# Performance work log

Hardware: AMD Instinct MI355X
Metric: run time of the kernel (lower is better)

## Reference

```python
import jax, jax.numpy as jnp
import numpy as np

EPS = 1e-8  # torch F.cosine_similarity norm clamp
TEMPERATURE = 0.05


def setup_inputs() -> dict:
    key = jax.random.key(0)
    k1, k2 = jax.random.split(key)
    N, D = 8192, 768
    query_embeddings = jax.random.normal(k1, (N, D), dtype=jnp.float32)
    content_embeddings = jax.random.normal(k2, (N, D), dtype=jnp.float32)
    return {"query_embeddings": query_embeddings, "content_embeddings": content_embeddings}


def reference(query_embeddings, content_embeddings):
    # cosine_similarity(q[:,None], c[None,:], dim=2) == normalize(q) @ normalize(c).T
    qn = query_embeddings / jnp.maximum(
        jnp.linalg.norm(query_embeddings, axis=-1, keepdims=True), EPS)
    cn = content_embeddings / jnp.maximum(
        jnp.linalg.norm(content_embeddings, axis=-1, keepdims=True), EPS)
    sim = jnp.einsum('nd,md->nm', qn, cn) / TEMPERATURE  # [N, N]
    # cross-entropy with targets = arange(N): positive is the diagonal
    logz = jax.nn.logsumexp(sim, axis=-1)                # [N]
    loss = jnp.mean(logz - jnp.diagonal(sim))
    return loss
```

## Files before the change

kernel.cpp:

```cpp
#include <hip/hip_runtime.h>
#include <hip/hip_bf16.h>


#define NROWS 8192
#define DDIM  768
#define ROWB  1536
#define FROWB 3072
#define BK 64
#define NKT  (DDIM / BK)
#define NIT  (NKT / 2)
#define GRID_T (NROWS / 256)

constexpr float INV_TEMP = 20.0f;
constexpr float NORM_EPS = 1e-8f;

using bf16 = __hip_bfloat16;
typedef __attribute__((ext_vector_type(4))) float  f32x4;
typedef __attribute__((ext_vector_type(8))) short  bf16x8;

__global__ void norm_diag_kernel(const float* __restrict__ q, const float* __restrict__ c,
                                 bf16* __restrict__ qn, bf16* __restrict__ cn,
                                 float* __restrict__ diag) {
    int row = blockIdx.x, t = threadIdx.x;
    const float4* qv = (const float4*)(q + (size_t)row * DDIM);
    const float4* cv = (const float4*)(c + (size_t)row * DDIM);
    float4 a = qv[t], b = cv[t];
    float ssq = a.x * a.x + a.y * a.y + a.z * a.z + a.w * a.w;
    float ssc = b.x * b.x + b.y * b.y + b.z * b.z + b.w * b.w;
    float dot = a.x * b.x + a.y * b.y + a.z * b.z + a.w * b.w;
    #pragma unroll
    for (int m = 32; m; m >>= 1) {
        ssq += __shfl_xor(ssq, m);
        ssc += __shfl_xor(ssc, m);
        dot += __shfl_xor(dot, m);
    }
    __shared__ float w3[3][4];
    if ((t & 63) == 0) { w3[t >> 6][0] = ssq; w3[t >> 6][1] = ssc; w3[t >> 6][2] = dot; }
    __syncthreads();
    float SSQ = w3[0][0] + w3[1][0] + w3[2][0];
    float SSC = w3[0][1] + w3[1][1] + w3[2][1];
    float DOT = w3[0][2] + w3[1][2] + w3[2][2];
    float invq = 1.0f / fmaxf(sqrtf(SSQ), NORM_EPS);
    float invc = 1.0f / fmaxf(sqrtf(SSC), NORM_EPS);
    if (t == 0) diag[row] = DOT * invq * invc * INV_TEMP;
    union { ushort4 u; bf16 h[4]; } oq, oc;
    oq.h[0] = __float2bfloat16(a.x * invq); oq.h[1] = __float2bfloat16(a.y * invq);
    oq.h[2] = __float2bfloat16(a.z * invq); oq.h[3] = __float2bfloat16(a.w * invq);
    oc.h[0] = __float2bfloat16(b.x * invc); oc.h[1] = __float2bfloat16(b.y * invc);
    oc.h[2] = __float2bfloat16(b.z * invc); oc.h[3] = __float2bfloat16(b.w * invc);
    ((ushort4*)(qn + (size_t)row * DDIM))[t] = oq.u;
    ((ushort4*)(cn + (size_t)row * DDIM))[t] = oc.u;
}

__device__ __forceinline__ void async16(void* l, const void* g) {
    __builtin_amdgcn_global_load_lds(
        (const __attribute__((address_space(1))) void*)g,
        (__attribute__((address_space(3))) void*)l, 16, 0, 0);
}

#define BARRIER __builtin_amdgcn_s_barrier()
#define SCHED0  __builtin_amdgcn_sched_barrier(0)
#define PRIO1   __builtin_amdgcn_s_setprio(1)
#define PRIO0   __builtin_amdgcn_s_setprio(0)
#define LGKM0   do { asm volatile("s_waitcnt lgkmcnt(0)" ::: "memory"); SCHED0; } while (0)
#define VMCNT(n) do { asm volatile("s_waitcnt vmcnt(" #n ")" ::: "memory"); SCHED0; } while (0)

#define STAGE_A(P, H, KT) do {                                              \
    const char* _g = aG + (size_t)(H) * 128 * ROWB + (size_t)(KT) * 128;    \
    char* _l = lds + (P) * 65536 + (H) * 16384 + dstW;                      \
    async16(_l, _g);                                                        \
    async16(_l + 8192, _g + 64 * ROWB);                                     \
} while (0)
#define STAGE_B(P, H, KT) do {                                              \
    const char* _g = bG + (size_t)(H) * 128 * ROWB + (size_t)(KT) * 128;    \
    char* _l = lds + 32768 + (P) * 65536 + (H) * 16384 + dstW;              \
    async16(_l, _g);                                                        \
    async16(_l + 8192, _g + 64 * ROWB);                                     \
} while (0)

#define READ_A(P, MH) do {                                                  \
    const char* _ab = lds + (P) * 65536 + aBaseT + (MH) * 64 * 128;         \
    _Pragma("unroll") for (int mi = 0; mi < 4; ++mi) {                      \
        a[mi][0] = *(const bf16x8*)(_ab + mi * 2048 + xk0);                 \
        a[mi][1] = *(const bf16x8*)(_ab + mi * 2048 + xk1);                 \
    }                                                                       \
} while (0)
#define READ_B(P, NH) do {                                                  \
    const char* _bb = lds + 32768 + (P) * 65536 + bBaseT + (NH) * 32 * 128; \
    _Pragma("unroll") for (int ni = 0; ni < 2; ++ni) {                      \
        bfr[NH][ni][0] = *(const bf16x8*)(_bb + ni * 2048 + xk0);           \
        bfr[NH][ni][1] = *(const bf16x8*)(_bb + ni * 2048 + xk1);           \
    }                                                                       \
} while (0)

#define MFMA_Q(MH, NH)                                                      \
    _Pragma("unroll") for (int mi = 0; mi < 4; ++mi)                        \
    _Pragma("unroll") for (int ni = 0; ni < 2; ++ni) {                      \
        acc[(MH)*4+mi][(NH)*2+ni] = __builtin_amdgcn_mfma_f32_16x16x32_bf16(\
            a[mi][0], bfr[NH][ni][0], acc[(MH)*4+mi][(NH)*2+ni], 0, 0, 0);  \
        acc[(MH)*4+mi][(NH)*2+ni] = __builtin_amdgcn_mfma_f32_16x16x32_bf16(\
            a[mi][1], bfr[NH][ni][1], acc[(MH)*4+mi][(NH)*2+ni], 0, 0, 0);  \
    }

__launch_bounds__(512, 2)
__global__ void simgemm_kernel(const bf16* __restrict__ A, const bf16* __restrict__ B,
                               float* __restrict__ partial) {
    __shared__ __attribute__((aligned(16))) char smem[131072];
    char* lds = smem;

    const int bid = blockIdx.x;
    const int tm = bid >> 5, tn = bid & 31;
    const int rowBase = tm * 256, colBase = tn * 256;
    const int tid = threadIdx.x;
    const int wid = tid >> 6, lane = tid & 63;
    const int wr = wid >> 2, wc = wid & 3;

    const int sr  = tid >> 3;
    const int scb = ((tid & 7) * 16) ^ ((sr & 7) << 4);
    const char* aG = (const char*)A + (size_t)(rowBase + sr) * ROWB + scb;
    const char* bG = (const char*)B + (size_t)(colBase + sr) * ROWB + scb;
    const int dstW = wid * 1024;

    const int aBaseT = wr * 16384 + (lane & 15) * 128;
    const int bBaseT = (wc >> 1) * 16384 + ((wc & 1) * 64 + (lane & 15)) * 128;
    const int klane  = (lane >> 4) * 16;
    const int swz    = (lane & 7) << 4;
    const int xk0    = klane ^ swz;
    const int xk1    = (64 + klane) ^ swz;

    f32x4  acc[8][4] = {};
    bf16x8 a[4][2];
    bf16x8 bfr[2][2][2];

    STAGE_A(0, 0, 0); STAGE_A(0, 1, 0);
    STAGE_B(0, 0, 0); STAGE_B(0, 1, 0);
    STAGE_A(1, 0, 1); STAGE_A(1, 1, 1);
    VMCNT(4);
    BARRIER; SCHED0;

    for (int i = 0; i < NIT; ++i) {
        const int t1 = 2 * i + 1;
        const int t2 = 2 * i + 2, t3 = 2 * i + 3;
        const bool more = (i + 1 < NIT);
        READ_A(0, 0); READ_B(0, 0);
        STAGE_B(1, 0, t1);
        BARRIER; LGKM0; PRIO1; MFMA_Q(0, 0); PRIO0; BARRIER; SCHED0;
        READ_B(0, 1);
        STAGE_B(1, 1, t1);
        BARRIER; LGKM0; PRIO1; MFMA_Q(0, 1); PRIO0; BARRIER; SCHED0;
        READ_A(0, 1);
        if (more) STAGE_A(0, 0, t2);
        BARRIER; LGKM0; PRIO1; MFMA_Q(1, 0); PRIO0; BARRIER; SCHED0;
        if (more) STAGE_A(0, 1, t2);
        BARRIER; LGKM0; PRIO1; MFMA_Q(1, 1); PRIO0;
        if (more) { VMCNT(4); } else { VMCNT(0); }
        BARRIER; SCHED0;
        READ_A(1, 0); READ_B(1, 0);
        if (more) STAGE_B(0, 0, t2);
        BARRIER; LGKM0; PRIO1; MFMA_Q(0, 0); PRIO0; BARRIER; SCHED0;
        READ_B(1, 1);
        if (more) STAGE_B(0, 1, t2);
        BARRIER; LGKM0; PRIO1; MFMA_Q(0, 1); PRIO0; BARRIER; SCHED0;
        READ_A(1, 1);
        if (more) STAGE_A(1, 0, t3);
        BARRIER; LGKM0; PRIO1; MFMA_Q(1, 0); PRIO0; BARRIER; SCHED0;
        if (more) STAGE_A(1, 1, t3);
        BARRIER; LGKM0; PRIO1; MFMA_Q(1, 1); PRIO0;
        if (more) { VMCNT(4); }
        BARRIER; SCHED0;
    }

    __syncthreads();
    float* red = (float*)smem;
    #pragma unroll
    for (int m = 0; m < 8; ++m) {
        #pragma unroll
        for (int r = 0; r < 4; ++r) {
            float s = 0.f;
            #pragma unroll
            for (int n = 0; n < 4; ++n)
                s += __expf(fmaf(INV_TEMP, acc[m][n][r], -INV_TEMP));
            s += __shfl_xor(s, 1);
            s += __shfl_xor(s, 2);
            s += __shfl_xor(s, 4);
            s += __shfl_xor(s, 8);
            if ((lane & 15) == 0)
                red[(wr * 128 + m * 16 + (lane >> 4) * 4 + r) * 4 + wc] = s;
        }
    }
    __syncthreads();
    if (tid < 256)
        partial[(size_t)(rowBase + tid) * GRID_T + tn] =
            red[tid * 4 + 0] + red[tid * 4 + 1] + red[tid * 4 + 2] + red[tid * 4 + 3];
}

__global__ void finalize_kernel(const float* __restrict__ partial,
                                const float* __restrict__ diag,
                                float* __restrict__ out) {
    int row = blockIdx.x * 256 + threadIdx.x;
    const float4* p = (const float4*)(partial + (size_t)row * GRID_T);
    float z = 0.f;
    #pragma unroll
    for (int i = 0; i < GRID_T / 4; ++i) {
        float4 v = p[i];
        z += v.x + v.y + v.z + v.w;
    }
    float term = INV_TEMP + logf(z) - diag[row];
    #pragma unroll
    for (int m = 32; m; m >>= 1) term += __shfl_xor(term, m);
    __shared__ float wsum[4];
    if ((threadIdx.x & 63) == 0) wsum[threadIdx.x >> 6] = term;
    __syncthreads();
    if (threadIdx.x == 0) {
        float s = wsum[0] + wsum[1] + wsum[2] + wsum[3];
        atomicAdd(out, s * (1.0f / NROWS));
    }
}

extern "C" void kernel_launch(void* const* d_in, const int* in_sizes, int n_in,
                              void* d_out, int out_size, void* d_ws, size_t ws_size,
                              hipStream_t stream) {
    const float* q = (const float*)d_in[0];
    const float* c = (const float*)d_in[1];
    float* out = (float*)d_out;

    char* ws = (char*)d_ws;
    bf16* qn = (bf16*)ws;
    bf16* cn = (bf16*)(ws + (size_t)NROWS * DDIM * 2);
    float* diag = (float*)(ws + (size_t)NROWS * DDIM * 4);
    float* partial = diag + NROWS;

    hipMemsetAsync(d_out, 0, sizeof(float), stream);

    norm_diag_kernel<<<NROWS, 192, 0, stream>>>(q, c, qn, cn, diag);
    simgemm_kernel<<<GRID_T * GRID_T, 512, 0, stream>>>(qn, cn, partial);
    finalize_kernel<<<NROWS / 256, 256, 0, stream>>>(partial, diag, out);
}
```

Before: 193.3 us.

## Use wave-per-row normalization, swizzle GEMM tile order, drop explicit LDS waits

The normalization kernel now gives each 64-lane wave a full row (three float4 per lane), which removes the shared-memory reduction and __syncthreads. The GEMM remaps block IDs so that consecutive blocks cover an 8x4 group of output tiles, spread across XCDs, to improve L2 reuse of A and B tiles. The explicit s_waitcnt lgkmcnt(0) before each MFMA group is removed and the compiler is left to insert LDS waits. That could let MFMAs overlap LDS reads, but correctness then depends on the compiler placing the waits correctly across the sched_barriers.

```diff
diff --git a/kernel.cpp b/kernel.cpp
--- a/kernel.cpp
+++ b/kernel.cpp
@@ -5,9 +5,7 @@
 #define NROWS 8192
 #define DDIM  768
 #define ROWB  1536
-#define FROWB 3072
-#define BK 64
-#define NKT  (DDIM / BK)
+#define NKT  (DDIM / 64)
 #define NIT  (NKT / 2)
 #define GRID_T (NROWS / 256)
 
@@ -21,35 +19,41 @@
 __global__ void norm_diag_kernel(const float* __restrict__ q, const float* __restrict__ c,
                                  bf16* __restrict__ qn, bf16* __restrict__ cn,
                                  float* __restrict__ diag) {
-    int row = blockIdx.x, t = threadIdx.x;
+    const int row  = (blockIdx.x * 256 + threadIdx.x) >> 6;
+    const int lane = threadIdx.x & 63;
     const float4* qv = (const float4*)(q + (size_t)row * DDIM);
     const float4* cv = (const float4*)(c + (size_t)row * DDIM);
-    float4 a = qv[t], b = cv[t];
-    float ssq = a.x * a.x + a.y * a.y + a.z * a.z + a.w * a.w;
-    float ssc = b.x * b.x + b.y * b.y + b.z * b.z + b.w * b.w;
-    float dot = a.x * b.x + a.y * b.y + a.z * b.z + a.w * b.w;
+    float4 a[3], b[3];
+    #pragma unroll
+    for (int j = 0; j < 3; ++j) { a[j] = qv[lane + j * 64]; b[j] = cv[lane + j * 64]; }
+    float ssq = 0.f, ssc = 0.f, dot = 0.f;
+    #pragma unroll
+    for (int j = 0; j < 3; ++j) {
+        ssq += a[j].x * a[j].x + a[j].y * a[j].y + a[j].z * a[j].z + a[j].w * a[j].w;
+        ssc += b[j].x * b[j].x + b[j].y * b[j].y + b[j].z * b[j].z + b[j].w * b[j].w;
+        dot += a[j].x * b[j].x + a[j].y * b[j].y + a[j].z * b[j].z + a[j].w * b[j].w;
+    }
     #pragma unroll
     for (int m = 32; m; m >>= 1) {
         ssq += __shfl_xor(ssq, m);
         ssc += __shfl_xor(ssc, m);
         dot += __shfl_xor(dot, m);
     }
-    __shared__ float w3[3][4];
-    if ((t & 63) == 0) { w3[t >> 6][0] = ssq; w3[t >> 6][1] = ssc; w3[t >> 6][2] = dot; }
-    __syncthreads();
-    float SSQ = w3[0][0] + w3[1][0] + w3[2][0];
-    float SSC = w3[0][1] + w3[1][1] + w3[2][1];
-    float DOT = w3[0][2] + w3[1][2] + w3[2][2];
-    float invq = 1.0f / fmaxf(sqrtf(SSQ), NORM_EPS);
-    float invc = 1.0f / fmaxf(sqrtf(SSC), NORM_EPS);
-    if (t == 0) diag[row] = DOT * invq * invc * INV_TEMP;
-    union { ushort4 u; bf16 h[4]; } oq, oc;
-    oq.h[0] = __float2bfloat16(a.x * invq); oq.h[1] = __float2bfloat16(a.y * invq);
-    oq.h[2] = __float2bfloat16(a.z * invq); oq.h[3] = __float2bfloat16(a.w * invq);
-    oc.h[0] = __float2bfloat16(b.x * invc); oc.h[1] = __float2bfloat16(b.y * invc);
-    oc.h[2] = __float2bfloat16(b.z * invc); oc.h[3] = __float2bfloat16(b.w * invc);
-    ((ushort4*)(qn + (size_t)row * DDIM))[t] = oq.u;
-    ((ushort4*)(cn + (size_t)row * DDIM))[t] = oc.u;
+    float invq = 1.0f / fmaxf(sqrtf(ssq), NORM_EPS);
+    float invc = 1.0f / fmaxf(sqrtf(ssc), NORM_EPS);
+    if (lane == 0) diag[row] = dot * invq * invc * INV_TEMP;
+    ushort4* qo = (ushort4*)(qn + (size_t)row * DDIM);
+    ushort4* co = (ushort4*)(cn + (size_t)row * DDIM);
+    #pragma unroll
+    for (int j = 0; j < 3; ++j) {
+        union { ushort4 u; bf16 h[4]; } oq, oc;
+        oq.h[0] = __float2bfloat16(a[j].x * invq); oq.h[1] = __float2bfloat16(a[j].y * invq);
+        oq.h[2] = __float2bfloat16(a[j].z * invq); oq.h[3] = __float2bfloat16(a[j].w * invq);
+        oc.h[0] = __float2bfloat16(b[j].x * invc); oc.h[1] = __float2bfloat16(b[j].y * invc);
+        oc.h[2] = __float2bfloat16(b[j].z * invc); oc.h[3] = __float2bfloat16(b[j].w * invc);
+        qo[lane + j * 64] = oq.u;
+        co[lane + j * 64] = oc.u;
+    }
 }
 
 __device__ __forceinline__ void async16(void* l, const void* g) {
@@ -62,7 +66,6 @@
 #define SCHED0  __builtin_amdgcn_sched_barrier(0)
 #define PRIO1   __builtin_amdgcn_s_setprio(1)
 #define PRIO0   __builtin_amdgcn_s_setprio(0)
-#define LGKM0   do { asm volatile("s_waitcnt lgkmcnt(0)" ::: "memory"); SCHED0; } while (0)
 #define VMCNT(n) do { asm volatile("s_waitcnt vmcnt(" #n ")" ::: "memory"); SCHED0; } while (0)
 
 #define STAGE_A(P, H, KT) do {                                              \
@@ -109,7 +112,10 @@
     char* lds = smem;
 
     const int bid = blockIdx.x;
-    const int tm = bid >> 5, tn = bid & 31;
+    const int swz = (bid & 7) * 128 + (bid >> 3);
+    const int st = swz >> 5, within = swz & 31;
+    const int tm = (st >> 3) * 8 + (within & 7);
+    const int tn = (st & 7) * 4 + (within >> 3);
     const int rowBase = tm * 256, colBase = tn * 256;
     const int tid = threadIdx.x;
     const int wid = tid >> 6, lane = tid & 63;
@@ -124,9 +130,9 @@
     const int aBaseT = wr * 16384 + (lane & 15) * 128;
     const int bBaseT = (wc >> 1) * 16384 + ((wc & 1) * 64 + (lane & 15)) * 128;
     const int klane  = (lane >> 4) * 16;
-    const int swz    = (lane & 7) << 4;
-    const int xk0    = klane ^ swz;
-    const int xk1    = (64 + klane) ^ swz;
+    const int swzr   = (lane & 7) << 4;
+    const int xk0    = klane ^ swzr;
+    const int xk1    = (64 + klane) ^ swzr;
 
     f32x4  acc[8][4] = {};
     bf16x8 a[4][2];
@@ -144,28 +150,28 @@
         const bool more = (i + 1 < NIT);
         READ_A(0, 0); READ_B(0, 0);
         STAGE_B(1, 0, t1);
-        BARRIER; LGKM0; PRIO1; MFMA_Q(0, 0); PRIO0; BARRIER; SCHED0;
+        BARRIER; PRIO1; MFMA_Q(0, 0); PRIO0; BARRIER; SCHED0;
         READ_B(0, 1);
         STAGE_B(1, 1, t1);
-        BARRIER; LGKM0; PRIO1; MFMA_Q(0, 1); PRIO0; BARRIER; SCHED0;
+        BARRIER; PRIO1; MFMA_Q(0, 1); PRIO0; BARRIER; SCHED0;
         READ_A(0, 1);
         if (more) STAGE_A(0, 0, t2);
-        BARRIER; LGKM0; PRIO1; MFMA_Q(1, 0); PRIO0; BARRIER; SCHED0;
+        BARRIER; PRIO1; MFMA_Q(1, 0); PRIO0; BARRIER; SCHED0;
         if (more) STAGE_A(0, 1, t2);
-        BARRIER; LGKM0; PRIO1; MFMA_Q(1, 1); PRIO0;
+        BARRIER; PRIO1; MFMA_Q(1, 1); PRIO0;
         if (more) { VMCNT(4); } else { VMCNT(0); }
         BARRIER; SCHED0;
         READ_A(1, 0); READ_B(1, 0);
         if (more) STAGE_B(0, 0, t2);
-        BARRIER; LGKM0; PRIO1; MFMA_Q(0, 0); PRIO0; BARRIER; SCHED0;
+        BARRIER; PRIO1; MFMA_Q(0, 0); PRIO0; BARRIER; SCHED0;
         READ_B(1, 1);
         if (more) STAGE_B(0, 1, t2);
-        BARRIER; LGKM0; PRIO1; MFMA_Q(0, 1); PRIO0; BARRIER; SCHED0;
+        BARRIER; PRIO1; MFMA_Q(0, 1); PRIO0; BARRIER; SCHED0;
         READ_A(1, 1);
         if (more) STAGE_A(1, 0, t3);
-        BARRIER; LGKM0; PRIO1; MFMA_Q(1, 0); PRIO0; BARRIER; SCHED0;
+        BARRIER; PRIO1; MFMA_Q(1, 0); PRIO0; BARRIER; SCHED0;
         if (more) STAGE_A(1, 1, t3);
-        BARRIER; LGKM0; PRIO1; MFMA_Q(1, 1); PRIO0;
+        BARRIER; PRIO1; MFMA_Q(1, 1); PRIO0;
         if (more) { VMCNT(4); }
         BARRIER; SCHED0;
     }
@@ -232,7 +238,7 @@
 
     hipMemsetAsync(d_out, 0, sizeof(float), stream);
 
-    norm_diag_kernel<<<NROWS, 192, 0, stream>>>(q, c, qn, cn, diag);
+    norm_diag_kernel<<<NROWS / 4, 256, 0, stream>>>(q, c, qn, cn, diag);
     simgemm_kernel<<<GRID_T * GRID_T, 512, 0, stream>>>(qn, cn, partial);
     finalize_kernel<<<NROWS / 256, 256, 0, stream>>>(partial, diag, out);
 }
```

New measurement: 193.1 us. Within noise of the previous version (-0.1%).
